# Optimization experiments

Measured on AMD Instinct MI355X. Metric: run time of the kernel, lower is better.

## Reference

```python
import jax, jax.numpy as jnp
import numpy as np

E, C_IN, NUM_CLASSES = 4, 3, 100
HW = 32
C1, C2, GC = 64, 128, 16
FC_IN = C2 * (HW // 4) * (HW // 4)  # 128*8*8 = 8192


def _conv(x, w, b):
    # x: [B,Cin,H,W], w: [Cout,Cin,3,3] -> [B,Cout,H,W] (SAME padding)
    y = jax.lax.conv_general_dilated(x, w, (1, 1), 'SAME',
                                     dimension_numbers=('NCHW', 'OIHW', 'NCHW'))
    return y + b[None, :, None, None]


def _maxpool2(x):
    return jax.lax.reduce_window(x, -jnp.inf, jax.lax.max,
                                 (1, 1, 2, 2), (1, 1, 2, 2), 'VALID')


def setup_inputs() -> dict:
    key = jax.random.key(0)
    ks = jax.random.split(key, 12)
    s = lambda k, shape, fan: (jax.random.normal(k, shape, jnp.float32) / np.sqrt(fan))
    return {
        'x': jax.random.normal(ks[0], (1024, C_IN, HW, HW), jnp.float32),
        # gating network
        'gate_cw': s(ks[1], (GC, C_IN, 3, 3), C_IN * 9),
        'gate_cb': jnp.zeros((GC,), jnp.float32),
        'gate_fw': s(ks[2], (E, GC), GC),
        'gate_fb': jnp.zeros((E,), jnp.float32),
        # stacked expert params [E, ...]
        'e_c1w': s(ks[3], (E, C1, C_IN, 3, 3), C_IN * 9),
        'e_c1b': jnp.zeros((E, C1), jnp.float32),
        'e_c2w': s(ks[4], (E, C2, C1, 3, 3), C1 * 9),
        'e_c2b': jnp.zeros((E, C2), jnp.float32),
        'e_fw': s(ks[5], (E, NUM_CLASSES, FC_IN), FC_IN),
        'e_fb': jnp.zeros((E, NUM_CLASSES), jnp.float32),
    }


def reference(x, gate_cw, gate_cb, gate_fw, gate_fb,
              e_c1w, e_c1b, e_c2w, e_c2b, e_fw, e_fb):
    B = x.shape[0]
    # --- gating: conv -> relu -> global avg pool -> linear -> softmax ---
    g = jax.nn.relu(_conv(x, gate_cw, gate_cb))            # [B,GC,H,W]
    g = g.mean(axis=(2, 3))                                # [B,GC]
    router_probs = jax.nn.softmax(g @ gate_fw.T + gate_fb) # [B,E]

    best_weights = router_probs.max(axis=1)                # [B]
    best_indices = jnp.argmax(router_probs, axis=1)        # [B]

    # --- hard top-1 dispatch: mask-and-combine (same math as gather/scatter) ---
    final_output = jnp.zeros((B, NUM_CLASSES), x.dtype)
    for e in range(E):  # fixed small expert count, structurally distinct params
        h = jax.nn.relu(_conv(x, e_c1w[e], e_c1b[e]))      # [B,64,32,32]
        h = _maxpool2(h)                                   # [B,64,16,16]
        h = jax.nn.relu(_conv(h, e_c2w[e], e_c2b[e]))      # [B,128,16,16]
        h = _maxpool2(h)                                   # [B,128,8,8]
        logits = h.reshape(B, -1) @ e_fw[e].T + e_fb[e]    # [B,100]
        mask = (best_indices == e)[:, None]
        final_output = final_output + jnp.where(
            mask, logits * best_weights[:, None], 0.0)

    mean_probs = router_probs.mean(axis=0)
    aux_loss = jnp.mean((mean_probs - 1.0 / E) ** 2)
    return final_output, router_probs, aux_loss
```

## Files before the change

kernel.cpp:

```cpp
#include <hip/hip_runtime.h>
#include <hip/hip_bf16.h>
#include <cstdint>


#define B_TOT 1024

typedef __attribute__((ext_vector_type(8))) short short8;
typedef __attribute__((ext_vector_type(16))) float f32x16;

__device__ __forceinline__ ushort f2bf(float f) {
  uint32_t u = __float_as_uint(f);
  u += 0x7fffu + ((u >> 16) & 1u);
  return (ushort)(u >> 16);
}

__global__ __launch_bounds__(256) void k_wprep(const float* __restrict__ w2,
                                               ushort* __restrict__ wp) {
  const int i = blockIdx.x * 256 + threadIdx.x;
  const int j = i & 7;
  const int cout = (i >> 3) & 127;
  const int kb = (i >> 10) & 7;
  const int kkE = i >> 13;
  const int kk = kkE - (kkE / 9) * 9;
  const int e = kkE / 9;
  const int ci = kb * 8 + j;
  const float f = w2[(size_t)(((e * 128 + cout) * 64 + ci) * 9) + kk];
  wp[i] = f2bf(f);
}

__global__ __launch_bounds__(256) void k_w1prep(const float* __restrict__ w1,
                                                ushort* __restrict__ wA) {
  const int i = blockIdx.x * 256 + threadIdx.x;
  const int j = i & 7;
  const int cout = (i >> 3) & 63;
  const int kb = (i >> 9) & 3;
  const int e = i >> 11;
  const int k = kb * 8 + j;
  float f = 0.f;
  if (k < 27) {
    const int ci = k / 9;
    const int kk = k - ci * 9;
    f = w1[(size_t)(((e * 64 + cout) * 3 + ci) * 9) + kk];
  }
  wA[i] = f2bf(f);
}

__global__ __launch_bounds__(256) void k_wfc(const float* __restrict__ efw,
                                             ushort* __restrict__ wfc) {
  const int i = blockIdx.x * 256 + threadIdx.x;
  const int j = i & 7;
  const int cout = (i >> 3) & 127;
  const int kb = (i >> 10) & 1023;
  const int e = i >> 20;
  const int k = kb * 8 + j;
  float f = 0.f;
  if (cout < 100) f = efw[((size_t)(e * 100 + cout)) * 8192 + k];
  wfc[i] = f2bf(f);
}

__global__ __launch_bounds__(256, 2) void k_gate(
    const float* __restrict__ x, const float* __restrict__ gcw,
    const float* __restrict__ gcb, float* __restrict__ g_mean) {
  __shared__ float xs[3 * 34 * 34];
  __shared__ float red[4 * 16];
  const int b = blockIdx.x;
  const int t = threadIdx.x;
  const float* xb = x + (size_t)b * 3072;

  for (int c = t; c < 3468; c += 256) {
    const int ci = c / 1156;
    const int rem = c - ci * 1156;
    const int y = rem / 34;
    const int xx = rem - y * 34;
    const int gy = y - 1, gx = xx - 1;
    float v = 0.f;
    if (gy >= 0 && gy < 32 && gx >= 0 && gx < 32) v = xb[ci * 1024 + gy * 32 + gx];
    xs[c] = v;
  }
  __syncthreads();

  const int r = t >> 3;
  const int c0 = (t & 7) * 4;

  float accp[16][4];
#pragma unroll
  for (int c = 0; c < 16; c++)
#pragma unroll
    for (int p = 0; p < 4; p++) accp[c][p] = 0.f;

#pragma unroll
  for (int ci = 0; ci < 3; ci++) {
    float pv[3][6];
#pragma unroll
    for (int dy = 0; dy < 3; dy++) {
      const float* row = xs + ci * 1156 + (r + dy) * 34 + c0;
#pragma unroll
      for (int dx = 0; dx < 6; dx++) pv[dy][dx] = row[dx];
    }
#pragma unroll
    for (int c = 0; c < 16; c++) {
      const float* wr = gcw + (c * 3 + ci) * 9;
#pragma unroll
      for (int ky = 0; ky < 3; ky++)
#pragma unroll
        for (int kx = 0; kx < 3; kx++) {
          const float wv = wr[ky * 3 + kx];
#pragma unroll
          for (int p = 0; p < 4; p++)
            accp[c][p] += wv * pv[ky][kx + p];
        }
    }
  }

  float sums[16];
#pragma unroll
  for (int c = 0; c < 16; c++) {
    const float bb = gcb[c];
    float s = 0.f;
#pragma unroll
    for (int p = 0; p < 4; p++) s += fmaxf(accp[c][p] + bb, 0.f);
    sums[c] = s;
  }

  const int wave = t >> 6, lane = t & 63;
#pragma unroll
  for (int c = 0; c < 16; c++) {
    float v = sums[c];
    for (int o = 32; o > 0; o >>= 1) v += __shfl_down(v, o);
    if (lane == 0) red[wave * 16 + c] = v;
  }
  __syncthreads();
  if (t < 16) {
    g_mean[b * 16 + t] =
        (red[t] + red[16 + t] + red[32 + t] + red[48 + t]) * (1.f / 1024.f);
  }
}

__global__ __launch_bounds__(256) void k_router(
    const float* __restrict__ g_mean, const float* __restrict__ gfw,
    const float* __restrict__ gfb, float* __restrict__ probs,
    float* __restrict__ best_w, int* __restrict__ best_idx,
    int* __restrict__ counts) {
  const int b = blockIdx.x * 256 + threadIdx.x;
  float g[16];
#pragma unroll
  for (int c = 0; c < 16; c++) g[c] = g_mean[b * 16 + c];
  float lg[4];
#pragma unroll
  for (int e = 0; e < 4; e++) {
    float s = gfb[e];
#pragma unroll
    for (int c = 0; c < 16; c++) s += g[c] * gfw[e * 16 + c];
    lg[e] = s;
  }
  float m = fmaxf(fmaxf(lg[0], lg[1]), fmaxf(lg[2], lg[3]));
  float ex[4], s = 0.f;
#pragma unroll
  for (int e = 0; e < 4; e++) { ex[e] = expf(lg[e] - m); s += ex[e]; }
  const float inv = 1.f / s;
  float p[4];
#pragma unroll
  for (int e = 0; e < 4; e++) { p[e] = ex[e] * inv; probs[b * 4 + e] = p[e]; }
  int bi = 0; float bp = p[0];
#pragma unroll
  for (int e = 1; e < 4; e++) if (p[e] > bp) { bp = p[e]; bi = e; }
  best_w[b] = bp;
  best_idx[b] = bi;
  atomicAdd(&counts[bi], 1);
}

__global__ void k_offsets(const int* __restrict__ counts, int* __restrict__ off) {
  if (threadIdx.x == 0) {
    int o = 0;
    for (int e = 0; e < 4; e++) { off[e] = o; o += ((counts[e] + 31) & ~31); }
    off[4] = o;
  }
}

__global__ __launch_bounds__(256) void k_scatter(
    const int* __restrict__ best_idx, const int* __restrict__ off,
    int* __restrict__ cnt2, int* __restrict__ order) {
  const int b = blockIdx.x * 256 + threadIdx.x;
  const int e = best_idx[b];
  const int slot = off[e] + atomicAdd(&cnt2[e], 1);
  order[slot] = b;
}

__global__ __launch_bounds__(256) void k_aux(const float* __restrict__ probs,
                                             float* __restrict__ aux_out) {
  __shared__ float red[16];
  const int t = threadIdx.x;
  const int wave = t >> 6, lane = t & 63;
  float sums[4] = {0.f, 0.f, 0.f, 0.f};
  for (int b = t; b < B_TOT; b += 256) {
#pragma unroll
    for (int e = 0; e < 4; e++) sums[e] += probs[b * 4 + e];
  }
#pragma unroll
  for (int e = 0; e < 4; e++) {
    float v = sums[e];
    for (int o = 32; o > 0; o >>= 1) v += __shfl_down(v, o);
    if (lane == 0) red[wave * 4 + e] = v;
  }
  __syncthreads();
  if (t == 0) {
    float aux = 0.f;
#pragma unroll
    for (int e = 0; e < 4; e++) {
      const float mp = (red[e] + red[4 + e] + red[8 + e] + red[12 + e]) * (1.f / 1024.f);
      const float d = mp - 0.25f;
      aux += d * d;
    }
    aux_out[0] = aux * 0.25f;
  }
}

__global__ __launch_bounds__(256) void k_conv1(
    const float* __restrict__ x, const ushort* __restrict__ wA,
    const float* __restrict__ b1, const int* __restrict__ best_idx,
    ushort* __restrict__ h1q) {
  __shared__ ushort xs[1020];
  __shared__ __align__(16) ushort Bl[256 * 32];
  const int blk = blockIdx.x;
  const int b = blk >> 2;
  const int q = blk & 3;
  const int t = threadIdx.x;
  const int e = __builtin_amdgcn_readfirstlane(best_idx[b]);
  const float* xb = x + (size_t)b * 3072;
  const float* b1e = b1 + (size_t)e * 64;

  for (int c = t; c < 1020; c += 256) {
    const int ci = c / 340;
    const int rem = c - ci * 340;
    const int hr = rem / 34;
    const int hc = rem - hr * 34;
    const int gr = 8 * q + hr - 1, gc = hc - 1;
    float v = 0.f;
    if (gr >= 0 && gr < 32 && gc >= 0 && gc < 32) v = xb[ci * 1024 + gr * 32 + gc];
    xs[c] = f2bf(v);
  }
  __syncthreads();

  {
    const int rr = t >> 5, cc = t & 31;
    ushort us[32];
#pragma unroll
    for (int k = 0; k < 32; k++) {
      ushort v = 0;
      if (k < 27) {
        const int ci = k / 9;
        const int tap = k - ci * 9;
        const int dy = tap / 3, dx = tap - dy * 3;
        v = xs[ci * 340 + (rr + dy) * 34 + cc + dx];
      }
      us[k] = v;
    }
    uint4 pk[2];
    uint* pu = (uint*)pk;
#pragma unroll
    for (int w = 0; w < 8; w++)
      pu[w] = (uint)us[w * 2] | ((uint)us[w * 2 + 1] << 16);
    *(uint4*)(Bl + t * 32) = pk[0];
    *(uint4*)(Bl + t * 32 + 8) = pk[1];
    uint4 pk2[2];
    uint* pu2 = (uint*)pk2;
#pragma unroll
    for (int w = 0; w < 8; w++)
      pu2[w] = (uint)us[16 + w * 2] | ((uint)us[16 + w * 2 + 1] << 16);
    *(uint4*)(Bl + t * 32 + 16) = pk2[0];
    *(uint4*)(Bl + t * 32 + 24) = pk2[1];
  }
  __syncthreads();

  const int lane = t & 63;
  const int wv = t >> 6;
  const int g = wv & 1;
  const int nh = wv >> 1;
  const int ln = lane & 31;
  const int half = lane >> 5;

  const short8 af0 = *(const short8*)(wA + (size_t)(((e * 4 + half) * 64) + g * 32 + ln) * 8);
  const short8 af1 = *(const short8*)(wA + (size_t)(((e * 4 + 2 + half) * 64) + g * 32 + ln) * 8);

  f32x16 acc[4];
#pragma unroll
  for (int tt = 0; tt < 4; tt++)
#pragma unroll
    for (int i = 0; i < 16; i++) acc[tt][i] = 0.f;

#pragma unroll
  for (int tt = 0; tt < 4; tt++) {
    const ushort* bcol = Bl + (size_t)((nh * 4 + tt) * 32 + ln) * 32;
    const short8 b0 = *(const short8*)(bcol + half * 8);
    const short8 b1v = *(const short8*)(bcol + 16 + half * 8);
    acc[tt] = __builtin_amdgcn_mfma_f32_32x32x16_bf16(af0, b0, acc[tt], 0, 0, 0);
    acc[tt] = __builtin_amdgcn_mfma_f32_32x32x16_bf16(af1, b1v, acc[tt], 0, 0, 0);
  }

  float bias[16];
#pragma unroll
  for (int r = 0; r < 16; r++)
    bias[r] = b1e[g * 32 + (r & 3) + 8 * (r >> 2) + 4 * half];

  const int pc = ln >> 1;
#pragma unroll
  for (int j = 0; j < 2; j++) {
    float pw[16];
#pragma unroll
    for (int r = 0; r < 16; r++) {
      float v = fmaxf(acc[2 * j][r], acc[2 * j + 1][r]);
      v = fmaxf(v, __shfl_xor(v, 1));
      pw[r] = fmaxf(v + bias[r], 0.f);
    }
    if ((lane & 1) == 0) {
      const int pos = (4 * q + nh * 2 + j) * 16 + pc;
      ushort* dst = h1q + (size_t)b * 16384 + pos * 8 + 4 * half;
#pragma unroll
      for (int rg = 0; rg < 4; rg++) {
        uint2 pk;
        pk.x = (uint)f2bf(pw[rg * 4 + 0]) | ((uint)f2bf(pw[rg * 4 + 1]) << 16);
        pk.y = (uint)f2bf(pw[rg * 4 + 2]) | ((uint)f2bf(pw[rg * 4 + 3]) << 16);
        *(uint2*)(dst + (g * 4 + rg) * 2048) = pk;
      }
    }
  }
}

__global__ __launch_bounds__(256) void k_conv2(
    const ushort* __restrict__ h1q, const ushort* __restrict__ wp,
    const float* __restrict__ b2, const int* __restrict__ best_idx,
    ushort* __restrict__ h2q) {
  __shared__ uint4 st[864];
  __shared__ float pl[2048];
  const int blk = blockIdx.x;
  const int b = blk >> 2;
  const int yq = blk & 3;
  const int t = threadIdx.x;
  const int e = __builtin_amdgcn_readfirstlane(best_idx[b]);

  for (int c = t; c < 864; c += 256) {
    const int row = c / 144;
    const int rem = c - row * 144;
    const int cig = rem / 18;
    const int col = rem - cig * 18;
    const int gy = yq * 4 - 1 + row;
    uint4 v = make_uint4(0u, 0u, 0u, 0u);
    if (gy >= 0 && gy < 16 && col >= 1 && col <= 16)
      v = *(const uint4*)(h1q + (size_t)b * 16384 + cig * 2048 +
                          (gy * 16 + col - 1) * 8);
    st[c] = v;
  }
  __syncthreads();

  const int wv = t >> 6;
  const int g = wv & 1;
  const int h = wv >> 1;
  const int lane = t & 63;
  const int n = lane & 31;
  const int half = lane >> 5;
  const int drow = n >> 4;
  const int col = n & 15;
  const int cm0 = g * 64;

  f32x16 acc0, acc1;
#pragma unroll
  for (int i = 0; i < 16; i++) { acc0[i] = 0.f; acc1[i] = 0.f; }

  const ushort* wpe = wp + (size_t)e * 73728;
  const short* sb = (const short*)st;

  for (int kk = 0; kk < 9; kk++) {
    const int ky = kk / 3;
    const int kx = kk - ky * 3;
#pragma unroll
    for (int c4 = 0; c4 < 4; c4++) {
      const int cig = c4 * 2 + half;
      const short8 af0 = *(const short8*)(wpe + kk * 8192 +
                                          (size_t)(cig * 128 + cm0 + n) * 8);
      const short8 af1 = *(const short8*)(wpe + kk * 8192 +
                                          (size_t)(cig * 128 + cm0 + 32 + n) * 8);
      const short8 bf = *(const short8*)(sb +
          (((2 * h + drow + ky) * 8 + cig) * 18 + col + kx) * 8);
      acc0 = __builtin_amdgcn_mfma_f32_32x32x16_bf16(af0, bf, acc0, 0, 0, 0);
      acc1 = __builtin_amdgcn_mfma_f32_32x32x16_bf16(af1, bf, acc1, 0, 0, 0);
    }
  }

#pragma unroll
  for (int s = 0; s < 2; s++) {
    const f32x16 a = s ? acc1 : acc0;
#pragma unroll
    for (int r = 0; r < 16; r++) {
      float v = a[r];
      v = fmaxf(v, __shfl_xor(v, 1));
      v = fmaxf(v, __shfl_xor(v, 16));
      if ((lane & 17) == 0) {
        const int rowm = (r & 3) + 8 * (r >> 2) + 4 * half;
        const int pc = (n >> 1) & 7;
        pl[(cm0 + s * 32 + rowm) * 16 + h * 8 + pc] = v;
      }
    }
  }
  __syncthreads();

  {
    const int coutL = t >> 1;
    const int hh = t & 1;
    const float bias = b2[e * 128 + coutL];
    const float* src = pl + coutL * 16 + hh * 8;
    union { ushort us[8]; uint4 u4; } pk;
#pragma unroll
    for (int j = 0; j < 8; j++) pk.us[j] = f2bf(fmaxf(src[j] + bias, 0.f));
    *(uint4*)(h2q + (size_t)b * 8192 + coutL * 64 + yq * 16 + hh * 8) = pk.u4;
  }
}

__global__ __launch_bounds__(256) void k_fc(
    const ushort* __restrict__ h2q, const ushort* __restrict__ wfc,
    const int* __restrict__ order, const int* __restrict__ off,
    const int* __restrict__ counts, float* __restrict__ partial) {
  __shared__ ushort bs[32 * 32 * 8];
  __shared__ int sid[32];
  const int tix = blockIdx.x;
  const int ks = blockIdx.y;
  const int base = tix * 32;
  if (base >= off[4]) return;
  int e = 0;
#pragma unroll
  for (int i = 1; i < 4; i++) if (base >= off[i]) e = i;
  const int vend = off[e] + counts[e];
  const int t = threadIdx.x;
  if (t < 32) {
    const int pos = base + t;
    sid[t] = (pos < vend) ? order[pos] : -1;
  }
  __syncthreads();

  const int lane = t & 63;
  const int wv = t >> 6;
  const int half = lane >> 5;
  const int mn = lane & 31;
  const int cout0 = wv * 32;
  const int ss = t & 31;
  const int kgrp = t >> 5;
  const int srow = sid[ss] >= 0 ? sid[ss] : 0;
  const ushort* arow = h2q + (size_t)srow * 8192;

  f32x16 acc;
#pragma unroll
  for (int i = 0; i < 16; i++) acc[i] = 0.f;

  const ushort* wbase = wfc + ((size_t)e * 1024 + (size_t)ks * 64) * 1024;
  const short* sb = (const short*)bs;

#pragma unroll
  for (int ch = 0; ch < 2; ch++) {
    const int k0g = ks * 512 + ch * 256;
    if (ch) __syncthreads();
#pragma unroll
    for (int p = 0; p < 4; p++) {
      const int kb = p * 8 + kgrp;
      const uint4 v = *(const uint4*)(arow + k0g + kb * 8);
      *(uint4*)(bs + (kb * 32 + ss) * 8) = v;
    }
    __syncthreads();
#pragma unroll
    for (int kk = 0; kk < 16; kk++) {
      const int kbl = kk * 2 + half;
      const short8 af = *(const short8*)(wbase +
          ((size_t)(ch * 32 + kbl) * 128 + cout0 + mn) * 8);
      const short8 bf = *(const short8*)(sb + (kbl * 32 + mn) * 8);
      acc = __builtin_amdgcn_mfma_f32_32x32x16_bf16(af, bf, acc, 0, 0, 0);
    }
  }

  float* pks = partial + (size_t)ks * 147456;
#pragma unroll
  for (int r = 0; r < 16; r++) {
    const int cout = cout0 + (r & 3) + 8 * (r >> 2) + 4 * half;
    pks[(size_t)cout * 1152 + base + mn] = acc[r];
  }
}

__global__ __launch_bounds__(256) void k_red(
    const float* __restrict__ partial, const float* __restrict__ efb,
    const int* __restrict__ order, const int* __restrict__ off,
    const int* __restrict__ counts, const float* __restrict__ best_w,
    float* __restrict__ out) {
  const int slot = blockIdx.x * 256 + threadIdx.x;
  if (slot >= off[4]) return;
  int e = 0;
#pragma unroll
  for (int i = 1; i < 4; i++) if (slot >= off[i]) e = i;
  if (slot - off[e] >= counts[e]) return;
  const int s = order[slot];
  const float bw = best_w[s];
  const int o0 = blockIdx.y * 4;
#pragma unroll
  for (int j = 0; j < 4; j++) {
    const int o = o0 + j;
    float sum = 0.f;
#pragma unroll
    for (int ks = 0; ks < 16; ks++)
      sum += partial[(size_t)ks * 147456 + (size_t)o * 1152 + slot];
    out[(size_t)s * 100 + o] = (sum + efb[e * 100 + o]) * bw;
  }
}

extern "C" void kernel_launch(void* const* d_in, const int* in_sizes, int n_in,
                              void* d_out, int out_size, void* d_ws, size_t ws_size,
                              hipStream_t stream) {
  const float* x   = (const float*)d_in[0];
  const float* gcw = (const float*)d_in[1];
  const float* gcb = (const float*)d_in[2];
  const float* gfw = (const float*)d_in[3];
  const float* gfb = (const float*)d_in[4];
  const float* c1w = (const float*)d_in[5];
  const float* c1b = (const float*)d_in[6];
  const float* c2w = (const float*)d_in[7];
  const float* c2b = (const float*)d_in[8];
  const float* efw = (const float*)d_in[9];
  const float* efb = (const float*)d_in[10];
  float* out = (float*)d_out;
  float* ws  = (float*)d_ws;

  float*  g_mean   = ws;
  float*  best_w   = ws + 16384;
  int*    best_idx = (int*)(ws + 17408);
  int*    counts   = (int*)(ws + 18432);
  int*    cnt2     = (int*)(ws + 18436);
  int*    off      = (int*)(ws + 18440);
  int*    order    = (int*)(ws + 18448);
  ushort* wp       = (ushort*)(ws + 20480);
  ushort* wfc      = (ushort*)(ws + 167936);
  ushort* h1       = (ushort*)(ws + 2265088);
  ushort* h2q      = (ushort*)(ws + 10653696);
  float*  partial  = ws + 14848000;
  ushort* wA       = (ushort*)(ws + 17207296);

  float* probs = out + 102400;
  float* aux   = out + 106496;

  hipMemsetAsync(counts, 0, 8 * sizeof(int), stream);

  k_wprep<<<1152, 256, 0, stream>>>(c2w, wp);
  k_w1prep<<<128, 256, 0, stream>>>(c1w, wA);
  k_wfc<<<16384, 256, 0, stream>>>(efw, wfc);
  k_gate<<<1024, 256, 0, stream>>>(x, gcw, gcb, g_mean);
  k_router<<<4, 256, 0, stream>>>(g_mean, gfw, gfb, probs, best_w, best_idx, counts);
  k_offsets<<<1, 64, 0, stream>>>(counts, off);
  k_scatter<<<4, 256, 0, stream>>>(best_idx, off, cnt2, order);
  k_aux<<<1, 256, 0, stream>>>(probs, aux);
  k_conv1<<<4096, 256, 0, stream>>>(x, wA, c1b, best_idx, h1);
  k_conv2<<<4096, 256, 0, stream>>>(h1, wp, c2b, best_idx, h2q);
  dim3 g5(36, 16);
  k_fc<<<g5, 256, 0, stream>>>(h2q, wfc, order, off, counts, partial);
  dim3 g6(5, 25);
  k_red<<<g6, 256, 0, stream>>>(partial, efb, order, off, counts, best_w, out);
}
```

Measured before the change: 252.1 us.

## Process whole image per conv2 block to reuse weight fragments across row tiles

The conv2 kernel now handles a full 16x16 image per block instead of a quarter, staging the whole padded input in shared memory. Each weight fragment load now feeds four MFMA column tiles, so per-image weight traffic drops and halo rows are no longer reloaded. The epilogue applies bias, ReLU and bf16 packing before writing to shared memory, then does one coalesced copy out. In exchange each block holds 8 accumulator tiles (more registers) and uses more LDS, and the grid shrinks from 4096 to 1024 blocks, which may lower occupancy.

```diff
diff --git a/kernel.cpp b/kernel.cpp
--- a/kernel.cpp
+++ b/kernel.cpp
@@ -330,88 +330,93 @@
     const ushort* __restrict__ h1q, const ushort* __restrict__ wp,
     const float* __restrict__ b2, const int* __restrict__ best_idx,
     ushort* __restrict__ h2q) {
-  __shared__ uint4 st[864];
-  __shared__ float pl[2048];
-  const int blk = blockIdx.x;
-  const int b = blk >> 2;
-  const int yq = blk & 3;
+  __shared__ uint4 st[2592];
+  const int b = blockIdx.x;
   const int t = threadIdx.x;
   const int e = __builtin_amdgcn_readfirstlane(best_idx[b]);
-
-  for (int c = t; c < 864; c += 256) {
+  const ushort* wpe = wp + (size_t)e * 73728;
+
+  for (int c = t; c < 2592; c += 256) {
     const int row = c / 144;
     const int rem = c - row * 144;
     const int cig = rem / 18;
     const int col = rem - cig * 18;
-    const int gy = yq * 4 - 1 + row;
+    const int gy = row - 1, gx = col - 1;
     uint4 v = make_uint4(0u, 0u, 0u, 0u);
-    if (gy >= 0 && gy < 16 && col >= 1 && col <= 16)
-      v = *(const uint4*)(h1q + (size_t)b * 16384 + cig * 2048 +
-                          (gy * 16 + col - 1) * 8);
+    if (gy >= 0 && gy < 16 && gx >= 0 && gx < 16)
+      v = *(const uint4*)(h1q + (size_t)b * 16384 + cig * 2048 + (gy * 16 + gx) * 8);
     st[c] = v;
   }
   __syncthreads();
 
+  const int lane = t & 63;
   const int wv = t >> 6;
   const int g = wv & 1;
   const int h = wv >> 1;
-  const int lane = t & 63;
+  const int half = lane >> 5;
   const int n = lane & 31;
-  const int half = lane >> 5;
   const int drow = n >> 4;
-  const int col = n & 15;
+  const int col15 = n & 15;
   const int cm0 = g * 64;
 
-  f32x16 acc0, acc1;
-#pragma unroll
-  for (int i = 0; i < 16; i++) { acc0[i] = 0.f; acc1[i] = 0.f; }
-
-  const ushort* wpe = wp + (size_t)e * 73728;
-  const short* sb = (const short*)st;
+  f32x16 acc[2][4];
+#pragma unroll
+  for (int m = 0; m < 2; m++)
+#pragma unroll
+    for (int nt = 0; nt < 4; nt++)
+#pragma unroll
+      for (int i = 0; i < 16; i++) acc[m][nt][i] = 0.f;
+
+  const short* sbs = (const short*)st;
 
   for (int kk = 0; kk < 9; kk++) {
     const int ky = kk / 3;
     const int kx = kk - ky * 3;
 #pragma unroll
     for (int c4 = 0; c4 < 4; c4++) {
-      const int cig = c4 * 2 + half;
+      const int kb = c4 * 2 + half;
       const short8 af0 = *(const short8*)(wpe + kk * 8192 +
-                                          (size_t)(cig * 128 + cm0 + n) * 8);
+                                          (size_t)(kb * 128 + cm0 + n) * 8);
       const short8 af1 = *(const short8*)(wpe + kk * 8192 +
-                                          (size_t)(cig * 128 + cm0 + 32 + n) * 8);
-      const short8 bf = *(const short8*)(sb +
-          (((2 * h + drow + ky) * 8 + cig) * 18 + col + kx) * 8);
-      acc0 = __builtin_amdgcn_mfma_f32_32x32x16_bf16(af0, bf, acc0, 0, 0, 0);
-      acc1 = __builtin_amdgcn_mfma_f32_32x32x16_bf16(af1, bf, acc1, 0, 0, 0);
-    }
-  }
-
-#pragma unroll
-  for (int s = 0; s < 2; s++) {
-    const f32x16 a = s ? acc1 : acc0;
-#pragma unroll
-    for (int r = 0; r < 16; r++) {
-      float v = a[r];
-      v = fmaxf(v, __shfl_xor(v, 1));
-      v = fmaxf(v, __shfl_xor(v, 16));
-      if ((lane & 17) == 0) {
-        const int rowm = (r & 3) + 8 * (r >> 2) + 4 * half;
-        const int pc = (n >> 1) & 7;
-        pl[(cm0 + s * 32 + rowm) * 16 + h * 8 + pc] = v;
+                                          (size_t)(kb * 128 + cm0 + 32 + n) * 8);
+#pragma unroll
+      for (int nt = 0; nt < 4; nt++) {
+        const int rin = 8 * h + 2 * nt + drow + ky;
+        const int cin = col15 + kx;
+        const short8 bf = *(const short8*)(sbs + ((rin * 8 + kb) * 18 + cin) * 8);
+        acc[0][nt] = __builtin_amdgcn_mfma_f32_32x32x16_bf16(af0, bf, acc[0][nt], 0, 0, 0);
+        acc[1][nt] = __builtin_amdgcn_mfma_f32_32x32x16_bf16(af1, bf, acc[1][nt], 0, 0, 0);
       }
     }
   }
   __syncthreads();
 
+  ushort* pls = (ushort*)st;
+#pragma unroll
+  for (int m = 0; m < 2; m++)
+#pragma unroll
+    for (int nt = 0; nt < 4; nt++) {
+#pragma unroll
+      for (int r = 0; r < 16; r++) {
+        float v = acc[m][nt][r];
+        v = fmaxf(v, __shfl_xor(v, 1));
+        v = fmaxf(v, __shfl_xor(v, 16));
+        if ((lane & 17) == 0) {
+          const int rowm = (r & 3) + 8 * (r >> 2) + 4 * half;
+          const int cout = cm0 + m * 32 + rowm;
+          const int pr = 4 * h + nt;
+          const int pc = (n >> 1) & 7;
+          pls[cout * 64 + pr * 8 + pc] = f2bf(fmaxf(v + b2[e * 128 + cout], 0.f));
+        }
+      }
+    }
+  __syncthreads();
+
   {
-    const int coutL = t >> 1;
-    const int hh = t & 1;
-    const float bias = b2[e * 128 + coutL];
-    const float* src = pl + coutL * 16 + hh * 8;
-    union { ushort us[8]; uint4 u4; } pk;
-#pragma unroll
-    for (int j = 0; j < 8; j++) pk.us[j] = f2bf(fmaxf(src[j] + bias, 0.f));
-    *(uint4*)(h2q + (size_t)b * 8192 + coutL * 64 + yq * 16 + hh * 8) = pk.u4;
+    const uint4* srcv = (const uint4*)pls;
+    uint4* dstv = (uint4*)(h2q + (size_t)b * 8192);
+#pragma unroll
+    for (int p = 0; p < 4; p++) dstv[p * 256 + t] = srcv[p * 256 + t];
   }
 }
 
@@ -552,7 +557,7 @@
   k_scatter<<<4, 256, 0, stream>>>(best_idx, off, cnt2, order);
   k_aux<<<1, 256, 0, stream>>>(probs, aux);
   k_conv1<<<4096, 256, 0, stream>>>(x, wA, c1b, best_idx, h1);
-  k_conv2<<<4096, 256, 0, stream>>>(h1, wp, c2b, best_idx, h2q);
+  k_conv2<<<1024, 256, 0, stream>>>(h1, wp, c2b, best_idx, h2q);
   dim3 g5(36, 16);
   k_fc<<<g5, 256, 0, stream>>>(h2q, wfc, order, off, counts, partial);
   dim3 g6(5, 25);
```

After: 317.2 us. 25.8% more time.
